# Kernel optimization log

Hardware: AMD Instinct MI355X
Metric: run time of the kernel (lower is better)

The kernel has to match this reference:

```python
import jax, jax.numpy as jnp
import numpy as np

TAU = 0.1
MASK_VAL = 1e9


def setup_inputs() -> dict:
    key = jax.random.key(0)
    ka, kb = jax.random.split(key)
    B, D = 4096, 512
    return {
        "view_a": jax.random.normal(ka, (B, D), dtype=jnp.float32),
        "view_b": jax.random.normal(kb, (B, D), dtype=jnp.float32),
    }


def _l2norm(x):
    return x / jnp.maximum(jnp.linalg.norm(x, axis=-1, keepdims=True), 1e-12)


def reference(view_a, view_b):
    a = _l2norm(view_a)
    b = _l2norm(view_b)
    B = a.shape[0]
    labels = jnp.arange(B)  # start_i = 0 (single device)
    mask = jnp.eye(B, dtype=a.dtype) * MASK_VAL

    logits_aa = a @ a.T / TAU - mask
    logits_bb = b @ b.T / TAU - mask
    logits_ab = a @ b.T / TAU
    logits_ba = b @ a.T / TAU

    full_a = jnp.concatenate([logits_ab, logits_aa], axis=1)  # [B, 2B]
    full_b = jnp.concatenate([logits_ba, logits_bb], axis=1)

    def ce(logits):
        logp = jax.nn.log_softmax(logits, axis=-1)
        return -jnp.mean(jnp.take_along_axis(logp, labels[:, None], axis=-1))

    loss = (ce(full_a) + ce(full_b)) / 2

    pred = jnp.argmax(full_a, axis=-1)
    acc = 100.0 * jnp.sum(pred == labels) / B
    return loss, acc
```

## Files before the change

### kernel.cpp

```cpp
#include <hip/hip_runtime.h>
#include <stdint.h>


#define BN 4096
#define DK 512
#define NSPLIT 16
#define NEG_BIG -1e30f
#define SCL 0.15625f
#define SCL2 0.225396744f
#define C2 14.4269504f
#define TILE_BYTES (64 * DK)

typedef __attribute__((ext_vector_type(16))) float floatx16;
typedef __attribute__((ext_vector_type(8))) int intx8;

__global__ void __launch_bounds__(256) prep_kernel(
    const float* __restrict__ A, const float* __restrict__ Bv,
    unsigned char* __restrict__ An, unsigned char* __restrict__ Bn,
    float* __restrict__ diag, float* __restrict__ out) {
  if (blockIdx.x == 0 && threadIdx.x < 2) out[threadIdx.x] = 0.0f;
  const int w = threadIdx.x >> 6, lane = threadIdx.x & 63;
  const int row = blockIdx.x * 4 + w;
  const float4* pa4 = (const float4*)(A + (size_t)row * DK);
  const float4* pb4 = (const float4*)(Bv + (size_t)row * DK);
  float4 a0 = pa4[lane * 2], a1 = pa4[lane * 2 + 1];
  float4 b0 = pb4[lane * 2], b1 = pb4[lane * 2 + 1];
  float ssa = a0.x * a0.x + a0.y * a0.y + a0.z * a0.z + a0.w * a0.w +
              a1.x * a1.x + a1.y * a1.y + a1.z * a1.z + a1.w * a1.w;
  float ssb = b0.x * b0.x + b0.y * b0.y + b0.z * b0.z + b0.w * b0.w +
              b1.x * b1.x + b1.y * b1.y + b1.z * b1.z + b1.w * b1.w;
  float sab = a0.x * b0.x + a0.y * b0.y + a0.z * b0.z + a0.w * b0.w +
              a1.x * b1.x + a1.y * b1.y + a1.z * b1.z + a1.w * b1.w;
#pragma unroll
  for (int off = 32; off > 0; off >>= 1) {
    ssa += __shfl_xor(ssa, off);
    ssb += __shfl_xor(ssb, off);
    sab += __shfl_xor(sab, off);
  }
  float na = fmaxf(sqrtf(ssa), 1e-12f);
  float nb = fmaxf(sqrtf(ssb), 1e-12f);
  const float s = 8.0f;
  float sa = s / na, sb = s / nb;
  const int doff = (lane >> 2) * 32 + (lane & 1) * 16 + ((lane >> 1) & 1) * 8;
  {
    int v0 = __builtin_amdgcn_cvt_pk_fp8_f32(a0.x * sa, a0.y * sa, 0, false);
    v0 = __builtin_amdgcn_cvt_pk_fp8_f32(a0.z * sa, a0.w * sa, v0, true);
    int v1 = __builtin_amdgcn_cvt_pk_fp8_f32(a1.x * sa, a1.y * sa, 0, false);
    v1 = __builtin_amdgcn_cvt_pk_fp8_f32(a1.z * sa, a1.w * sa, v1, true);
    int2 pv; pv.x = v0; pv.y = v1;
    *(int2*)(An + (size_t)row * DK + doff) = pv;
  }
  {
    int v0 = __builtin_amdgcn_cvt_pk_fp8_f32(b0.x * sb, b0.y * sb, 0, false);
    v0 = __builtin_amdgcn_cvt_pk_fp8_f32(b0.z * sb, b0.w * sb, v0, true);
    int v1 = __builtin_amdgcn_cvt_pk_fp8_f32(b1.x * sb, b1.y * sb, 0, false);
    v1 = __builtin_amdgcn_cvt_pk_fp8_f32(b1.z * sb, b1.w * sb, v1, true);
    int2 pv; pv.x = v0; pv.y = v1;
    *(int2*)(Bn + (size_t)row * DK + doff) = pv;
  }
  if (lane == 0) diag[row] = (sab / (na * nb)) * 10.0f;
}

__global__ void __launch_bounds__(256, 2) tiles_kernel(
    const unsigned char* __restrict__ An, const unsigned char* __restrict__ Bn,
    float* __restrict__ pSA, float* __restrict__ pMA, float* __restrict__ pSB) {
  __shared__ __align__(16) unsigned char smem[2 * TILE_BYTES];

  const int rb = blockIdx.x;
  const int split = blockIdx.y;
  const int tid = threadIdx.x;
  const int lane = tid & 63, w = tid >> 6;
  const int n5 = lane & 31, h = lane >> 5;
  const int r0 = rb * 128;
  const int myrow = r0 + w * 32 + n5;

  intx8 aw[8];
  auto loadfrags = [&](const unsigned char* base) {
    const unsigned char* p = base + (size_t)myrow * DK + h * 16;
#pragma unroll
    for (int i = 0; i < 8; ++i) {
      int4 c0 = *(const int4*)(p + i * 64);
      int4 c1 = *(const int4*)(p + i * 64 + 32);
      intx8 v = {c0.x, c0.y, c0.z, c0.w, c1.x, c1.y, c1.z, c1.w};
      aw[i] = v;
    }
  };

  float l[16], mx[16];
#pragma unroll
  for (int r = 0; r < 16; ++r) { l[r] = 0.f; mx[r] = NEG_BIG; }

  auto stage = [&](unsigned char* buf, int jt) {
    const unsigned char* csrc = (jt < 64) ? An : Bn;
    const int cb = (jt & 63) * 64;
#pragma unroll
    for (int ii = 0; ii < 8; ++ii) {
      const int cp = w * 8 + ii;
      const int cl = cp * 2 + h;
      const unsigned char* src =
          csrc + (size_t)(cb + cl) * DK + ((n5 ^ (cl & 7)) * 16);
      __builtin_amdgcn_global_load_lds(
          (const __attribute__((address_space(1))) void*)src,
          (__attribute__((address_space(3))) void*)(buf + cp * 1024),
          16, 0, 0);
    }
  };

  stage(smem, split * 8);
  loadfrags(An);
  __syncthreads();

  const int swz = n5 & 7;
  for (int u = 0; u < 16; ++u) {
    const int t = u & 7;
    const int jt = split * 8 + t;
    unsigned char* cur = smem + (u & 1) * TILE_BYTES;
    unsigned char* nxt = smem + ((u + 1) & 1) * TILE_BYTES;
    if (u < 15) stage(nxt, split * 8 + ((t + 1) & 7));

    floatx16 acc[2];
#pragma unroll
    for (int cs = 0; cs < 2; ++cs)
#pragma unroll
      for (int r = 0; r < 16; ++r) acc[cs][r] = 0.f;

    const unsigned char* bbase = cur + (size_t)n5 * DK;
#pragma unroll
    for (int i = 0; i < 8; ++i) {
      const int p1 = ((4 * i + h) ^ swz) * 16;
      const int p2 = ((4 * i + 2 + h) ^ swz) * 16;
#pragma unroll
      for (int cs = 0; cs < 2; ++cs) {
        int4 b0 = *(const int4*)(bbase + cs * 32 * DK + p1);
        int4 b1 = *(const int4*)(bbase + cs * 32 * DK + p2);
        intx8 bw = {b0.x, b0.y, b0.z, b0.w, b1.x, b1.y, b1.z, b1.w};
        acc[cs] = __builtin_amdgcn_mfma_scale_f32_32x32x64_f8f6f4(
            aw[i], bw, acc[cs], 0, 0, 0, 0x7F7F7F7F, 0, 0x7F7F7F7F);
      }
    }

    const bool dtile = (((jt & 63) >> 1) == rb);
    const int colbase = (jt & 63) * 64;
    const bool passA = (u < 8);
#pragma unroll
    for (int r = 0; r < 16; ++r) {
      float v0 = acc[0][r], v1 = acc[1][r];
      if (dtile) {
        const int rowg = r0 + w * 32 + (r & 3) + 8 * (r >> 2) + 4 * h;
        if (rowg == colbase + n5)      v0 = NEG_BIG;
        if (rowg == colbase + 32 + n5) v1 = NEG_BIG;
      }
      if (passA) mx[r] = fmaxf(mx[r], fmaxf(v0, v1));
      l[r] += exp2f(fmaf(v0, SCL2, -C2)) + exp2f(fmaf(v1, SCL2, -C2));
    }

    if (u == 7) {
#pragma unroll
      for (int off = 1; off < 32; off <<= 1)
#pragma unroll
        for (int r = 0; r < 16; ++r) {
          l[r] += __shfl_xor(l[r], off);
          mx[r] = fmaxf(mx[r], __shfl_xor(mx[r], off));
        }
      if (n5 == 0) {
#pragma unroll
        for (int r = 0; r < 16; ++r) {
          const int row = r0 + w * 32 + (r & 3) + 8 * (r >> 2) + 4 * h;
          pSA[split * BN + row] = l[r];
          pMA[split * BN + row] = mx[r] * SCL;
        }
      }
#pragma unroll
      for (int r = 0; r < 16; ++r) l[r] = 0.f;
      loadfrags(Bn);
    }
    __syncthreads();
  }

#pragma unroll
  for (int off = 1; off < 32; off <<= 1)
#pragma unroll
    for (int r = 0; r < 16; ++r) l[r] += __shfl_xor(l[r], off);
  if (n5 == 0) {
#pragma unroll
    for (int r = 0; r < 16; ++r) {
      const int row = r0 + w * 32 + (r & 3) + 8 * (r >> 2) + 4 * h;
      pSB[split * BN + row] = l[r];
    }
  }
}

__global__ void __launch_bounds__(256) finalize_kernel(
    const float* __restrict__ pSA, const float* __restrict__ pMA,
    const float* __restrict__ pSB, const float* __restrict__ diag,
    float* __restrict__ out) {
  const int row = blockIdx.x * 256 + threadIdx.x;
  float SA = 0.f, SB = 0.f, MA = NEG_BIG;
#pragma unroll
  for (int s = 0; s < NSPLIT; ++s) {
    SA += pSA[s * BN + row];
    SB += pSB[s * BN + row];
    MA = fmaxf(MA, pMA[s * BN + row]);
  }
  const float d = diag[row];
  const float eL = exp2f(fmaf(d, 1.44269504f, -C2));
  float lseA = 10.0f + logf(SA + eL);
  float lseB = 10.0f + logf(SB + eL);
  float lossi = (lseA - d) + (lseB - d);
  float corr = (d >= MA) ? 1.f : 0.f;
#pragma unroll
  for (int off = 32; off > 0; off >>= 1) {
    lossi += __shfl_xor(lossi, off);
    corr += __shfl_xor(corr, off);
  }
  __shared__ float sred[2][4];
  if ((threadIdx.x & 63) == 0) {
    int w = threadIdx.x >> 6;
    sred[0][w] = lossi; sred[1][w] = corr;
  }
  __syncthreads();
  if (threadIdx.x == 0) {
    float ls = sred[0][0] + sred[0][1] + sred[0][2] + sred[0][3];
    float cs = sred[1][0] + sred[1][1] + sred[1][2] + sred[1][3];
    atomicAdd(&out[0], ls * (1.0f / 8192.0f));
    atomicAdd(&out[1], cs * (100.0f / 4096.0f));
  }
}

extern "C" void kernel_launch(void* const* d_in, const int* in_sizes, int n_in,
                              void* d_out, int out_size, void* d_ws, size_t ws_size,
                              hipStream_t stream) {
  const float* A = (const float*)d_in[0];
  const float* Bv = (const float*)d_in[1];
  unsigned char* An = (unsigned char*)d_ws;
  unsigned char* Bn = An + (size_t)BN * DK;
  float* diag = (float*)(Bn + (size_t)BN * DK);
  float* pSA = diag + BN;
  float* pMA = pSA + NSPLIT * BN;
  float* pSB = pMA + NSPLIT * BN;
  float* out = (float*)d_out;

  prep_kernel<<<BN / 4, 256, 0, stream>>>(A, Bv, An, Bn, diag, out);
  tiles_kernel<<<dim3(32, 16), 256, 0, stream>>>(An, Bn, pSA, pMA, pSB);
  finalize_kernel<<<BN / 256, 256, 0, stream>>>(pSA, pMA, pSB, diag, out);
}
```

Baseline: 123.0 us.

## Reuse each staged column tile for both A and B row fragments

Instead of two sequential passes that each stream the same 64-column tiles (one pass with A-row fragments, one with B-row fragments), the kernel keeps both A and B row fragments in registers. It streams 32-column tiles once, issuing two MFMAs per LDS-read B fragment. This halves global-to-LDS staging traffic and LDS reads per MFMA, and halves the shared-memory buffer size. In exchange it doubles the register-resident fragment footprint and keeps three sets of running accumulators, which may raise register pressure at the two-blocks-per-CU launch bound.

After: 124.1 us. About the same (+0.9%).

```diff
diff --git a/kernel.cpp b/kernel.cpp
--- a/kernel.cpp
+++ b/kernel.cpp
@@ -9,7 +9,7 @@
 #define SCL 0.15625f
 #define SCL2 0.225396744f
 #define C2 14.4269504f
-#define TILE_BYTES (64 * DK)
+#define TILE_BYTES (32 * DK)
 
 typedef __attribute__((ext_vector_type(16))) float floatx16;
 typedef __attribute__((ext_vector_type(8))) int intx8;
@@ -74,28 +74,33 @@
   const int r0 = rb * 128;
   const int myrow = r0 + w * 32 + n5;
 
-  intx8 aw[8];
-  auto loadfrags = [&](const unsigned char* base) {
-    const unsigned char* p = base + (size_t)myrow * DK + h * 16;
+  intx8 awA[8], awB[8];
+  {
+    const unsigned char* pA = An + (size_t)myrow * DK + h * 16;
+    const unsigned char* pB = Bn + (size_t)myrow * DK + h * 16;
 #pragma unroll
     for (int i = 0; i < 8; ++i) {
-      int4 c0 = *(const int4*)(p + i * 64);
-      int4 c1 = *(const int4*)(p + i * 64 + 32);
+      int4 c0 = *(const int4*)(pA + i * 64);
+      int4 c1 = *(const int4*)(pA + i * 64 + 32);
       intx8 v = {c0.x, c0.y, c0.z, c0.w, c1.x, c1.y, c1.z, c1.w};
-      aw[i] = v;
-    }
-  };
-
-  float l[16], mx[16];
-#pragma unroll
-  for (int r = 0; r < 16; ++r) { l[r] = 0.f; mx[r] = NEG_BIG; }
+      awA[i] = v;
+      c0 = *(const int4*)(pB + i * 64);
+      c1 = *(const int4*)(pB + i * 64 + 32);
+      intx8 u = {c0.x, c0.y, c0.z, c0.w, c1.x, c1.y, c1.z, c1.w};
+      awB[i] = u;
+    }
+  }
+
+  float lA[16], lB[16], mx[16];
+#pragma unroll
+  for (int r = 0; r < 16; ++r) { lA[r] = 0.f; lB[r] = 0.f; mx[r] = NEG_BIG; }
 
   auto stage = [&](unsigned char* buf, int jt) {
-    const unsigned char* csrc = (jt < 64) ? An : Bn;
-    const int cb = (jt & 63) * 64;
-#pragma unroll
-    for (int ii = 0; ii < 8; ++ii) {
-      const int cp = w * 8 + ii;
+    const unsigned char* csrc = (jt < 128) ? An : Bn;
+    const int cb = (jt & 127) * 32;
+#pragma unroll
+    for (int ii = 0; ii < 4; ++ii) {
+      const int cp = w * 4 + ii;
       const int cl = cp * 2 + h;
       const unsigned char* src =
           csrc + (size_t)(cb + cl) * DK + ((n5 ^ (cl & 7)) * 16);
@@ -106,73 +111,46 @@
     }
   };
 
-  stage(smem, split * 8);
-  loadfrags(An);
+  stage(smem, split * 16);
   __syncthreads();
 
   const int swz = n5 & 7;
   for (int u = 0; u < 16; ++u) {
-    const int t = u & 7;
-    const int jt = split * 8 + t;
+    const int jt = split * 16 + u;
     unsigned char* cur = smem + (u & 1) * TILE_BYTES;
     unsigned char* nxt = smem + ((u + 1) & 1) * TILE_BYTES;
-    if (u < 15) stage(nxt, split * 8 + ((t + 1) & 7));
-
-    floatx16 acc[2];
-#pragma unroll
-    for (int cs = 0; cs < 2; ++cs)
-#pragma unroll
-      for (int r = 0; r < 16; ++r) acc[cs][r] = 0.f;
+    if (u < 15) stage(nxt, jt + 1);
+
+    floatx16 accA, accB;
+#pragma unroll
+    for (int r = 0; r < 16; ++r) { accA[r] = 0.f; accB[r] = 0.f; }
 
     const unsigned char* bbase = cur + (size_t)n5 * DK;
 #pragma unroll
     for (int i = 0; i < 8; ++i) {
       const int p1 = ((4 * i + h) ^ swz) * 16;
       const int p2 = ((4 * i + 2 + h) ^ swz) * 16;
-#pragma unroll
-      for (int cs = 0; cs < 2; ++cs) {
-        int4 b0 = *(const int4*)(bbase + cs * 32 * DK + p1);
-        int4 b1 = *(const int4*)(bbase + cs * 32 * DK + p2);
-        intx8 bw = {b0.x, b0.y, b0.z, b0.w, b1.x, b1.y, b1.z, b1.w};
-        acc[cs] = __builtin_amdgcn_mfma_scale_f32_32x32x64_f8f6f4(
-            aw[i], bw, acc[cs], 0, 0, 0, 0x7F7F7F7F, 0, 0x7F7F7F7F);
-      }
-    }
-
-    const bool dtile = (((jt & 63) >> 1) == rb);
-    const int colbase = (jt & 63) * 64;
-    const bool passA = (u < 8);
+      int4 b0 = *(const int4*)(bbase + p1);
+      int4 b1 = *(const int4*)(bbase + p2);
+      intx8 bw = {b0.x, b0.y, b0.z, b0.w, b1.x, b1.y, b1.z, b1.w};
+      accA = __builtin_amdgcn_mfma_scale_f32_32x32x64_f8f6f4(
+          awA[i], bw, accA, 0, 0, 0, 0x7F7F7F7F, 0, 0x7F7F7F7F);
+      accB = __builtin_amdgcn_mfma_scale_f32_32x32x64_f8f6f4(
+          awB[i], bw, accB, 0, 0, 0, 0x7F7F7F7F, 0, 0x7F7F7F7F);
+    }
+
+    const bool dtile = (((jt & 127) >> 2) == rb);
+    const int colbase = (jt & 127) * 32;
 #pragma unroll
     for (int r = 0; r < 16; ++r) {
-      float v0 = acc[0][r], v1 = acc[1][r];
+      float vA = accA[r], vB = accB[r];
       if (dtile) {
         const int rowg = r0 + w * 32 + (r & 3) + 8 * (r >> 2) + 4 * h;
-        if (rowg == colbase + n5)      v0 = NEG_BIG;
-        if (rowg == colbase + 32 + n5) v1 = NEG_BIG;
+        if (rowg == colbase + n5) { vA = NEG_BIG; vB = NEG_BIG; }
       }
-      if (passA) mx[r] = fmaxf(mx[r], fmaxf(v0, v1));
-      l[r] += exp2f(fmaf(v0, SCL2, -C2)) + exp2f(fmaf(v1, SCL2, -C2));
-    }
-
-    if (u == 7) {
-#pragma unroll
-      for (int off = 1; off < 32; off <<= 1)
-#pragma unroll
-        for (int r = 0; r < 16; ++r) {
-          l[r] += __shfl_xor(l[r], off);
-          mx[r] = fmaxf(mx[r], __shfl_xor(mx[r], off));
-        }
-      if (n5 == 0) {
-#pragma unroll
-        for (int r = 0; r < 16; ++r) {
-          const int row = r0 + w * 32 + (r & 3) + 8 * (r >> 2) + 4 * h;
-          pSA[split * BN + row] = l[r];
-          pMA[split * BN + row] = mx[r] * SCL;
-        }
-      }
-#pragma unroll
-      for (int r = 0; r < 16; ++r) l[r] = 0.f;
-      loadfrags(Bn);
+      mx[r] = fmaxf(mx[r], vA);
+      lA[r] += exp2f(fmaf(vA, SCL2, -C2));
+      lB[r] += exp2f(fmaf(vB, SCL2, -C2));
     }
     __syncthreads();
   }
@@ -180,12 +158,18 @@
 #pragma unroll
   for (int off = 1; off < 32; off <<= 1)
 #pragma unroll
-    for (int r = 0; r < 16; ++r) l[r] += __shfl_xor(l[r], off);
+    for (int r = 0; r < 16; ++r) {
+      lA[r] += __shfl_xor(lA[r], off);
+      lB[r] += __shfl_xor(lB[r], off);
+      mx[r] = fmaxf(mx[r], __shfl_xor(mx[r], off));
+    }
   if (n5 == 0) {
 #pragma unroll
     for (int r = 0; r < 16; ++r) {
       const int row = r0 + w * 32 + (r & 3) + 8 * (r >> 2) + 4 * h;
-      pSB[split * BN + row] = l[r];
+      pSA[split * BN + row] = lA[r];
+      pMA[split * BN + row] = mx[r] * SCL;
+      pSB[split * BN + row] = lB[r];
     }
   }
 }
```
